# Optimization experiments

Hardware: AMD Instinct MI355X
Metric: run time of the kernel (lower is better)

The kernel has to match this reference:

```python
import jax, jax.numpy as jnp
import numpy as np

NS, NC = 16, 8  # n_state, n_ctrl; n_sc = NS + NC


def setup_inputs() -> dict:
    key = jax.random.key(0)
    kQ, kp, kF, kc, kx = jax.random.split(key, 5)
    B, T, nsc = 512, 128, NS + NC
    Qr = jax.random.normal(kQ, (B, T, nsc, nsc), dtype=jnp.float32)
    # PSD + regularized so Quu is invertible (as in the torch example: Q = Q^T Q)
    Q = jnp.einsum('btji,btjk->btik', Qr, Qr) / nsc + jnp.eye(nsc, dtype=jnp.float32)
    p = jax.random.normal(kp, (B, T, nsc), dtype=jnp.float32)
    F = jax.random.normal(kF, (B, T, NS, nsc), dtype=jnp.float32) * 0.3
    c1 = jax.random.normal(kc, (B, T, NS), dtype=jnp.float32)
    x_init = jax.random.normal(kx, (B, NS), dtype=jnp.float32)
    return {"Q": Q, "p": p, "F": F, "c1": c1, "x_init": x_init}


def _lqr(Q, p, F, c1, x_init):
    B, T, nsc = Q.shape[0], Q.shape[1], Q.shape[2]
    ns = F.shape[2]
    # time-major for scan: [T, B, ...]
    Qt = jnp.moveaxis(Q, 1, 0)
    pt = jnp.moveaxis(p, 1, 0)
    Ft = jnp.moveaxis(F, 1, 0)
    ct = jnp.moveaxis(c1, 1, 0)

    def bwd(carry, inp):
        V, v = carry                       # [B,ns,ns], [B,ns]
        Qc, pc, Fc, cc = inp
        # Q_t + F^T V F ; q_t + F^T V c1 + F^T v
        Qh = Qc + jnp.einsum('bni,bnm,bmj->bij', Fc, V, Fc)
        qh = pc + jnp.einsum('bni,bnm,bm->bi', Fc, V, cc) + jnp.einsum('bni,bn->bi', Fc, v)
        Qxx = Qh[:, :ns, :ns]
        Qxu = Qh[:, :ns, ns:]
        Qux = Qh[:, ns:, :ns]
        Quu = Qh[:, ns:, ns:]
        qx = qh[:, :ns]
        qu = qh[:, ns:]
        K = -jnp.linalg.solve(Quu, Qux)                    # [B,nc,ns]
        k = -jnp.linalg.solve(Quu, qu[..., None])[..., 0]  # [B,nc]
        KtQuu = jnp.einsum('bci,bcd->bid', K, Quu)
        Vn = Qxx + Qxu @ K + jnp.einsum('bci,bcj->bij', K, Qux) + KtQuu @ K
        Vn = 0.5 * (Vn + jnp.swapaxes(Vn, -1, -2))
        vn = qx + jnp.einsum('bic,bc->bi', Qxu, k) \
             + jnp.einsum('bci,bc->bi', K, qu) + jnp.einsum('bid,bd->bi', KtQuu, k)
        return (Vn, vn), (K, k)

    V0 = jnp.zeros((B, ns, ns), Q.dtype)
    v0 = jnp.zeros((B, ns), Q.dtype)
    _, (Ks, ks) = jax.lax.scan(bwd, (V0, v0), (Qt, pt, Ft, ct), reverse=True)

    def fwd(x, inp):
        K, k, Fc, cc = inp
        u = jnp.einsum('bci,bi->bc', K, x) + k
        tau = jnp.concatenate([x, u], axis=-1)             # [B, nsc]
        x_next = jnp.einsum('bnj,bj->bn', Fc, tau) + cc
        return x_next, tau

    _, taus = jax.lax.scan(fwd, x_init, (Ks, ks, Ft, ct))
    return jnp.moveaxis(taus, 0, 1)                        # [B, T, nsc]


def reference(Q, p, F, c1, x_init):
    return _lqr(Q, p, F, c1, x_init)
```

## Files before the change

### kernel.cpp

```cpp
#include <hip/hip_runtime.h>

namespace {
constexpr int TT = 128;

__device__ __forceinline__ float rdlane(float v, int l) {
  return __int_as_float(__builtin_amdgcn_readlane(__float_as_int(v), l));
}

__device__ __forceinline__ void bsync() {
  asm volatile("s_waitcnt lgkmcnt(0)" ::: "memory");
  __builtin_amdgcn_s_barrier();
  asm volatile("" ::: "memory");
  __builtin_amdgcn_sched_barrier(0);
}

__global__ __launch_bounds__(256)
void lqr_kernel(const float* __restrict__ Qg, const float* __restrict__ pg,
                const float* __restrict__ Fg, const float* __restrict__ cg,
                const float* __restrict__ x0g, float* __restrict__ out)
{
  __shared__ __align__(16) float VT[16][20];
  __shared__ __align__(16) float vv[16];
  __shared__ __align__(16) float FTxd[2][25][20];
  __shared__ __align__(16) float WTx[25][20];
  __shared__ __align__(16) float QhT[25][36];
  __shared__ __align__(16) float Ks[TT][16][8];
  __shared__ __align__(16) float ksv[TT][8];

  const int tid  = threadIdx.x;
  const int lane = tid & 63;
  const int wv   = tid >> 6;
  const int b    = blockIdx.x;
  const size_t bt0 = (size_t)b * TT;

  const int jl = tid & 31;
  const int g  = tid >> 5;

  for (int e = tid; e < 320; e += 256) (&VT[0][0])[e] = 0.f;
  if (tid < 16) vv[tid] = 0.f;

  const int  fj   = tid >> 2, fk = tid & 3;
  const bool fact = (tid < 100);
  const int  fsw  = (fj < 24) ? ((fj >> 2) & 3) : 2;
  float Fr4[4] = {0.f, 0.f, 0.f, 0.f};

  auto loadF = [&](int t) {
    if (fact) {
      if (fj < 24) {
        const float* Fs = Fg + (bt0 + t) * 384 + fj;
        #pragma unroll
        for (int m = 0; m < 4; ++m) Fr4[m] = Fs[(4 * fk + m) * 24];
      } else {
        const float* cs = cg + (bt0 + t) * 16 + 4 * fk;
        #pragma unroll
        for (int m = 0; m < 4; ++m) Fr4[m] = cs[m];
      }
    }
  };
  auto commitF = [&](int buf) {
    if (fact) {
      float* dst = &FTxd[buf][fj][(fk ^ fsw) << 2];
      *(float4*)dst = make_float4(Fr4[0], Fr4[1], Fr4[2], Fr4[3]);
    }
  };

  float qreg[3] = {0.f, 0.f, 0.f}, qreg3 = 0.f;
  auto loadQ = [&](int t) {
    if (jl < 24) {
      const float* Qs = Qg + (bt0 + t) * 576;
      #pragma unroll
      for (int r = 0; r < 3; ++r) qreg[r] = Qs[(3 * g + r) * 24 + jl];
      if (g == 7) qreg3 = pg[(bt0 + t) * 24 + jl];
    }
  };

  loadF(TT - 1);
  loadQ(TT - 1);
  commitF((TT - 1) & 1);
  loadF(TT - 2);
  bsync();

  for (int t = TT - 1; t >= 0; --t) {
    const float* Fb = &FTxd[t & 1][0][0];

    float fr[16];
    if (jl < 25) {
      const int sj = (jl >> 2) & 3;
      const float* fb = Fb + jl * 20;
      #pragma unroll
      for (int q = 0; q < 4; ++q) {
        float4 v4 = *(const float4*)(fb + ((q ^ sj) << 2));
        fr[4*q+0] = v4.x; fr[4*q+1] = v4.y; fr[4*q+2] = v4.z; fr[4*q+3] = v4.w;
      }
      const int m0 = 2 * g, m1 = m0 + 1;
      float acc0 = (jl == 24) ? vv[m0] : 0.f;
      float acc1 = (jl == 24) ? vv[m1] : 0.f;
      #pragma unroll
      for (int q = 0; q < 4; ++q) {
        float4 a0 = *(const float4*)(&VT[m0][4*q]);
        float4 a1 = *(const float4*)(&VT[m1][4*q]);
        acc0 = fmaf(a0.x, fr[4*q+0], acc0); acc0 = fmaf(a0.y, fr[4*q+1], acc0);
        acc0 = fmaf(a0.z, fr[4*q+2], acc0); acc0 = fmaf(a0.w, fr[4*q+3], acc0);
        acc1 = fmaf(a1.x, fr[4*q+0], acc1); acc1 = fmaf(a1.y, fr[4*q+1], acc1);
        acc1 = fmaf(a1.z, fr[4*q+2], acc1); acc1 = fmaf(a1.w, fr[4*q+3], acc1);
      }
      float* wb = &WTx[0][0] + jl * 20;
      *(float2*)(wb + ((((g >> 1) ^ sj) << 2) + (m0 & 3))) = make_float2(acc0, acc1);
    }
    bsync();

    if (jl < 24) {
      #pragma unroll
      for (int r = 0; r < 3; ++r) {
        const int c = 3 * g + r;
        const int sc = (c >> 2) & 3;
        const float* wb = &WTx[0][0] + c * 20;
        float acc = qreg[r];
        #pragma unroll
        for (int q = 0; q < 4; ++q) {
          float4 w4 = *(const float4*)(wb + ((q ^ sc) << 2));
          acc = fmaf(w4.x, fr[4*q+0], acc); acc = fmaf(w4.y, fr[4*q+1], acc);
          acc = fmaf(w4.z, fr[4*q+2], acc); acc = fmaf(w4.w, fr[4*q+3], acc);
        }
        float* qb = &QhT[0][0] + c * 36;
        qb[(((jl >> 2) ^ sc) << 2) + (jl & 3)] = acc;
      }
      if (g == 7) {
        const float* wb = &WTx[0][0] + 24 * 20;
        float acc = qreg3;
        #pragma unroll
        for (int q = 0; q < 4; ++q) {
          float4 w4 = *(const float4*)(wb + ((q ^ 2) << 2));
          acc = fmaf(w4.x, fr[4*q+0], acc); acc = fmaf(w4.y, fr[4*q+1], acc);
          acc = fmaf(w4.z, fr[4*q+2], acc); acc = fmaf(w4.w, fr[4*q+3], acc);
        }
        float* qb = &QhT[0][0] + 24 * 36;
        qb[(((jl >> 2) ^ 2) << 2) + (jl & 3)] = acc;
      }
    }
    if (t > 0) loadQ(t - 1);
    bsync();

    const int gjw = 2 + (t & 1);
    if (wv == gjw) {
      __builtin_amdgcn_s_setprio(1);
      const int cl = (lane < 25) ? lane : 0;
      const int row = (cl < 8) ? (16 + cl) : ((cl < 24) ? (cl - 8) : 24);
      const int s = (row >> 2) & 3;
      const float* base = &QhT[0][0] + row * 36;
      float a_[8];
      {
        float4 x0v = *(const float4*)(base + ((4 ^ s) << 2));
        float4 x1v = *(const float4*)(base + ((5 ^ s) << 2));
        a_[0]=x0v.x; a_[1]=x0v.y; a_[2]=x0v.z; a_[3]=x0v.w;
        a_[4]=x1v.x; a_[5]=x1v.y; a_[6]=x1v.z; a_[7]=x1v.w;
      }
      #pragma unroll
      for (int pp = 0; pp < 8; ++pp) {
        float f_[8];
        f_[0] = rdlane(a_[0], pp); f_[1] = rdlane(a_[1], pp);
        f_[2] = rdlane(a_[2], pp); f_[3] = rdlane(a_[3], pp);
        f_[4] = rdlane(a_[4], pp); f_[5] = rdlane(a_[5], pp);
        f_[6] = rdlane(a_[6], pp); f_[7] = rdlane(a_[7], pp);
        float d = __builtin_amdgcn_rcpf(f_[pp]);
        a_[pp] *= d;
        #pragma unroll
        for (int r = 0; r < 8; ++r)
          if (r != pp) a_[r] = fmaf(-f_[r], a_[pp], a_[r]);
      }
      if (lane >= 8 && lane < 25) {
        float4 k0 = make_float4(-a_[0], -a_[1], -a_[2], -a_[3]);
        float4 k1 = make_float4(-a_[4], -a_[5], -a_[6], -a_[7]);
        float4* kp = (lane < 24) ? (float4*)&Ks[t][lane - 8][0] : (float4*)&ksv[t][0];
        kp[0] = k0; kp[1] = k1;
      }
      const int jv = lane & 31;
      const int ih = lane >> 5;
      const int sl = (jv < 16) ? (8 + jv) : 24;
      float xj[8];
      #pragma unroll
      for (int c = 0; c < 8; ++c)
        xj[c] = __int_as_float(
            __builtin_amdgcn_ds_bpermute(sl * 4, __float_as_int(a_[c])));
      if (jv < 16 || jv == 24) {
        const int row2 = (jv < 16) ? jv : 24;
        const int s3 = (row2 >> 2) & 3;
        const float* b2 = &QhT[0][0] + row2 * 36;
        const int q0 = 2 * ih, q1 = q0 + 1;
        float4 A0 = *(const float4*)(b2 + ((q0 ^ s3) << 2));
        float4 A1 = *(const float4*)(b2 + ((q1 ^ s3) << 2));
        float acc[8];
        acc[0]=A0.x; acc[1]=A0.y; acc[2]=A0.z; acc[3]=A0.w;
        acc[4]=A1.x; acc[5]=A1.y; acc[6]=A1.z; acc[7]=A1.w;
        #pragma unroll
        for (int c = 0; c < 8; ++c) {
          const int s2 = ((16 + c) >> 2) & 3;
          const float* qb = &QhT[0][0] + (16 + c) * 36;
          float4 B0 = *(const float4*)(qb + ((q0 ^ s2) << 2));
          float4 B1 = *(const float4*)(qb + ((q1 ^ s2) << 2));
          const float xc = xj[c];
          acc[0] = fmaf(-xc, B0.x, acc[0]); acc[1] = fmaf(-xc, B0.y, acc[1]);
          acc[2] = fmaf(-xc, B0.z, acc[2]); acc[3] = fmaf(-xc, B0.w, acc[3]);
          acc[4] = fmaf(-xc, B1.x, acc[4]); acc[5] = fmaf(-xc, B1.y, acc[5]);
          acc[6] = fmaf(-xc, B1.z, acc[6]); acc[7] = fmaf(-xc, B1.w, acc[7]);
        }
        float4* vp = (jv < 16) ? (float4*)&VT[jv][8 * ih] : (float4*)&vv[8 * ih];
        vp[0] = make_float4(acc[0], acc[1], acc[2], acc[3]);
        vp[1] = make_float4(acc[4], acc[5], acc[6], acc[7]);
      }
      __builtin_amdgcn_s_setprio(0);
    } else {
      if (t > 0) commitF((t - 1) & 1);
      if (t > 1) loadF(t - 2);
    }
    bsync();
  }

  if (wv != 0) return;

  float xv = (lane < 16) ? x0g[(size_t)b * 16 + lane] : 0.f;
  float xs_[16];
  #pragma unroll
  for (int i = 0; i < 16; ++i) xs_[i] = rdlane(xv, i);

  float FA[24], FB[24];
  float cA = 0.f, cB = 0.f;
  float KA[16], KB[16], kA = 0.f, kB = 0.f;

  auto loadFw = [&](int t, float (&Fr)[24], float& cr) {
    if (lane < 16) {
      const float* src = Fg + (bt0 + t) * 384 + lane * 24;
      #pragma unroll
      for (int r = 0; r < 6; ++r) {
        float4 f4v = ((const float4*)src)[r];
        Fr[4*r+0] = f4v.x; Fr[4*r+1] = f4v.y; Fr[4*r+2] = f4v.z; Fr[4*r+3] = f4v.w;
      }
      cr = cg[(bt0 + t) * 16 + lane];
    }
  };
  auto loadK = [&](int t, float (&K)[16], float& kk) {
    if (lane < 8) {
      #pragma unroll
      for (int i = 0; i < 16; ++i) K[i] = Ks[t][i][lane];
      kk = ksv[t][lane];
    }
  };

  auto fstep = [&](int t, const float (&Fr)[24], float cr,
                   const float (&K)[16], float kk) {
    float uv = 0.f;
    if (lane < 8) {
      float u0 = kk, u1 = 0.f;
      #pragma unroll
      for (int i = 0; i < 16; i += 2) {
        u0 = fmaf(K[i],     xs_[i],     u0);
        u1 = fmaf(K[i + 1], xs_[i + 1], u1);
      }
      uv = u0 + u1;
    }
    float us[8];
    #pragma unroll
    for (int c = 0; c < 8; ++c) us[c] = rdlane(uv, c);
    float* o = out + (bt0 + t) * 24;
    if (lane < 16) o[lane] = xv;
    if (lane < 8)  o[16 + lane] = uv;
    float x0a = cr, x1a = 0.f;
    #pragma unroll
    for (int j2 = 0; j2 < 16; j2 += 2) {
      x0a = fmaf(Fr[j2],     xs_[j2],     x0a);
      x1a = fmaf(Fr[j2 + 1], xs_[j2 + 1], x1a);
    }
    #pragma unroll
    for (int c = 0; c < 8; c += 2) {
      x0a = fmaf(Fr[16 + c],     us[c],     x0a);
      x1a = fmaf(Fr[16 + c + 1], us[c + 1], x1a);
    }
    xv = x0a + x1a;
    #pragma unroll
    for (int i = 0; i < 16; ++i) xs_[i] = rdlane(xv, i);
  };

  loadFw(0, FA, cA); loadK(0, KA, kA);
  for (int t = 0; t < TT; t += 2) {
    if (t + 1 < TT) { loadFw(t + 1, FB, cB); loadK(t + 1, KB, kB); }
    fstep(t, FA, cA, KA, kA);
    if (t + 2 < TT) { loadFw(t + 2, FA, cA); loadK(t + 2, KA, kA); }
    fstep(t + 1, FB, cB, KB, kB);
  }
}
}

extern "C" void kernel_launch(void* const* d_in, const int* in_sizes, int n_in,
                              void* d_out, int out_size, void* d_ws, size_t ws_size,
                              hipStream_t stream)
{
  (void)n_in; (void)out_size; (void)d_ws; (void)ws_size;
  const float* Q  = (const float*)d_in[0];
  const float* p  = (const float*)d_in[1];
  const float* F  = (const float*)d_in[2];
  const float* c1 = (const float*)d_in[3];
  const float* x0 = (const float*)d_in[4];
  float* outp = (float*)d_out;

  const int B = in_sizes[4] / 16;
  lqr_kernel<<<B, 256, 0, stream>>>(Q, p, F, c1, x0, outp);
}
```

Measured before the change: 282.9 us.

## Pack two batch chains per block with staggered phases sharing barriers

Each 512-thread block now processes two batch elements with separate shared-memory state. The second chain runs one phase behind the first, so the latency-bound Gauss-Jordan phase of one chain overlaps the matmul phases of the other within the same barrier intervals. The intent is to hide the serial per-timestep solve latency and halve the number of barrier rounds per batch. In exchange, shared memory per block roughly doubles, the grid is halved, and the extra skew adds one phase to the schedule; the code also assumes an even batch count.

Result: slower. 355.9 us (+25.8%).

```diff
diff --git a/kernel.cpp b/kernel.cpp
--- a/kernel.cpp
+++ b/kernel.cpp
@@ -14,35 +14,39 @@
   __builtin_amdgcn_sched_barrier(0);
 }
 
-__global__ __launch_bounds__(256)
+__global__ __launch_bounds__(512)
 void lqr_kernel(const float* __restrict__ Qg, const float* __restrict__ pg,
                 const float* __restrict__ Fg, const float* __restrict__ cg,
                 const float* __restrict__ x0g, float* __restrict__ out)
 {
-  __shared__ __align__(16) float VT[16][20];
-  __shared__ __align__(16) float vv[16];
-  __shared__ __align__(16) float FTxd[2][25][20];
-  __shared__ __align__(16) float WTx[25][20];
-  __shared__ __align__(16) float QhT[25][36];
-  __shared__ __align__(16) float Ks[TT][16][8];
-  __shared__ __align__(16) float ksv[TT][8];
+  __shared__ __align__(16) float VT[2][16][20];
+  __shared__ __align__(16) float vv[2][16];
+  __shared__ __align__(16) float FTxd[2][2][25][20];
+  __shared__ __align__(16) float WTx[2][25][20];
+  __shared__ __align__(16) float QhT[2][25][36];
+  __shared__ __align__(16) float Ks[2][TT][16][8];
+  __shared__ __align__(16) float ksv[2][TT][8];
 
   const int tid  = threadIdx.x;
-  const int lane = tid & 63;
-  const int wv   = tid >> 6;
-  const int b    = blockIdx.x;
-  const size_t bt0 = (size_t)b * TT;
-
-  const int jl = tid & 31;
-  const int g  = tid >> 5;
-
-  for (int e = tid; e < 320; e += 256) (&VT[0][0])[e] = 0.f;
-  if (tid < 16) vv[tid] = 0.f;
-
-  const int  fj   = tid >> 2, fk = tid & 3;
-  const bool fact = (tid < 100);
+  const int cid  = tid >> 8;
+  const int ctid = tid & 255;
+  const int lane = ctid & 63;
+  const int cwv  = ctid >> 6;
+  const int b2   = blockIdx.x * 2 + cid;
+  const size_t bt0 = (size_t)b2 * TT;
+
+  const int jl = ctid & 31;
+  const int g  = ctid >> 5;
+
+  for (int e = ctid; e < 320; e += 256) (&VT[cid][0][0])[e] = 0.f;
+  if (ctid < 16) vv[cid][ctid] = 0.f;
+
+  const int  fj   = ctid >> 2, fk = ctid & 3;
+  const bool fact = (ctid < 100);
   const int  fsw  = (fj < 24) ? ((fj >> 2) & 3) : 2;
   float Fr4[4] = {0.f, 0.f, 0.f, 0.f};
+  float qreg[3] = {0.f, 0.f, 0.f}, qreg3 = 0.f;
+  float fr[16];
 
   auto loadF = [&](int t) {
     if (fact) {
@@ -59,12 +63,10 @@
   };
   auto commitF = [&](int buf) {
     if (fact) {
-      float* dst = &FTxd[buf][fj][(fk ^ fsw) << 2];
+      float* dst = &FTxd[cid][buf][fj][(fk ^ fsw) << 2];
       *(float4*)dst = make_float4(Fr4[0], Fr4[1], Fr4[2], Fr4[3]);
     }
   };
-
-  float qreg[3] = {0.f, 0.f, 0.f}, qreg3 = 0.f;
   auto loadQ = [&](int t) {
     if (jl < 24) {
       const float* Qs = Qg + (bt0 + t) * 576;
@@ -74,16 +76,8 @@
     }
   };
 
-  loadF(TT - 1);
-  loadQ(TT - 1);
-  commitF((TT - 1) & 1);
-  loadF(TT - 2);
-  bsync();
-
-  for (int t = TT - 1; t >= 0; --t) {
-    const float* Fb = &FTxd[t & 1][0][0];
-
-    float fr[16];
+  auto phaseA = [&](int t) {
+    const float* Fb = &FTxd[cid][t & 1][0][0];
     if (jl < 25) {
       const int sj = (jl >> 2) & 3;
       const float* fb = Fb + jl * 20;
@@ -93,28 +87,29 @@
         fr[4*q+0] = v4.x; fr[4*q+1] = v4.y; fr[4*q+2] = v4.z; fr[4*q+3] = v4.w;
       }
       const int m0 = 2 * g, m1 = m0 + 1;
-      float acc0 = (jl == 24) ? vv[m0] : 0.f;
-      float acc1 = (jl == 24) ? vv[m1] : 0.f;
+      float acc0 = (jl == 24) ? vv[cid][m0] : 0.f;
+      float acc1 = (jl == 24) ? vv[cid][m1] : 0.f;
       #pragma unroll
       for (int q = 0; q < 4; ++q) {
-        float4 a0 = *(const float4*)(&VT[m0][4*q]);
-        float4 a1 = *(const float4*)(&VT[m1][4*q]);
+        float4 a0 = *(const float4*)(&VT[cid][m0][4*q]);
+        float4 a1 = *(const float4*)(&VT[cid][m1][4*q]);
         acc0 = fmaf(a0.x, fr[4*q+0], acc0); acc0 = fmaf(a0.y, fr[4*q+1], acc0);
         acc0 = fmaf(a0.z, fr[4*q+2], acc0); acc0 = fmaf(a0.w, fr[4*q+3], acc0);
         acc1 = fmaf(a1.x, fr[4*q+0], acc1); acc1 = fmaf(a1.y, fr[4*q+1], acc1);
         acc1 = fmaf(a1.z, fr[4*q+2], acc1); acc1 = fmaf(a1.w, fr[4*q+3], acc1);
       }
-      float* wb = &WTx[0][0] + jl * 20;
+      float* wb = &WTx[cid][0][0] + jl * 20;
       *(float2*)(wb + ((((g >> 1) ^ sj) << 2) + (m0 & 3))) = make_float2(acc0, acc1);
     }
-    bsync();
-
+  };
+
+  auto phaseB = [&](int t) {
     if (jl < 24) {
       #pragma unroll
       for (int r = 0; r < 3; ++r) {
         const int c = 3 * g + r;
         const int sc = (c >> 2) & 3;
-        const float* wb = &WTx[0][0] + c * 20;
+        const float* wb = &WTx[cid][0][0] + c * 20;
         float acc = qreg[r];
         #pragma unroll
         for (int q = 0; q < 4; ++q) {
@@ -122,11 +117,11 @@
           acc = fmaf(w4.x, fr[4*q+0], acc); acc = fmaf(w4.y, fr[4*q+1], acc);
           acc = fmaf(w4.z, fr[4*q+2], acc); acc = fmaf(w4.w, fr[4*q+3], acc);
         }
-        float* qb = &QhT[0][0] + c * 36;
+        float* qb = &QhT[cid][0][0] + c * 36;
         qb[(((jl >> 2) ^ sc) << 2) + (jl & 3)] = acc;
       }
       if (g == 7) {
-        const float* wb = &WTx[0][0] + 24 * 20;
+        const float* wb = &WTx[cid][0][0] + 24 * 20;
         float acc = qreg3;
         #pragma unroll
         for (int q = 0; q < 4; ++q) {
@@ -134,91 +129,116 @@
           acc = fmaf(w4.x, fr[4*q+0], acc); acc = fmaf(w4.y, fr[4*q+1], acc);
           acc = fmaf(w4.z, fr[4*q+2], acc); acc = fmaf(w4.w, fr[4*q+3], acc);
         }
-        float* qb = &QhT[0][0] + 24 * 36;
+        float* qb = &QhT[cid][0][0] + 24 * 36;
         qb[(((jl >> 2) ^ 2) << 2) + (jl & 3)] = acc;
       }
     }
     if (t > 0) loadQ(t - 1);
+  };
+
+  auto phaseG = [&](int tg) {
+    if (cwv != 2 + (tg & 1)) return;
+    __builtin_amdgcn_s_setprio(1);
+    const int cl = (lane < 25) ? lane : 0;
+    const int row = (cl < 8) ? (16 + cl) : ((cl < 24) ? (cl - 8) : 24);
+    const int s = (row >> 2) & 3;
+    const float* base = &QhT[cid][0][0] + row * 36;
+    float a_[8];
+    {
+      float4 x0v = *(const float4*)(base + ((4 ^ s) << 2));
+      float4 x1v = *(const float4*)(base + ((5 ^ s) << 2));
+      a_[0]=x0v.x; a_[1]=x0v.y; a_[2]=x0v.z; a_[3]=x0v.w;
+      a_[4]=x1v.x; a_[5]=x1v.y; a_[6]=x1v.z; a_[7]=x1v.w;
+    }
+    #pragma unroll
+    for (int pp = 0; pp < 8; ++pp) {
+      float f_[8];
+      f_[0] = rdlane(a_[0], pp); f_[1] = rdlane(a_[1], pp);
+      f_[2] = rdlane(a_[2], pp); f_[3] = rdlane(a_[3], pp);
+      f_[4] = rdlane(a_[4], pp); f_[5] = rdlane(a_[5], pp);
+      f_[6] = rdlane(a_[6], pp); f_[7] = rdlane(a_[7], pp);
+      float d = __builtin_amdgcn_rcpf(f_[pp]);
+      a_[pp] *= d;
+      #pragma unroll
+      for (int r = 0; r < 8; ++r)
+        if (r != pp) a_[r] = fmaf(-f_[r], a_[pp], a_[r]);
+    }
+    if (lane >= 8 && lane < 25) {
+      float4 k0 = make_float4(-a_[0], -a_[1], -a_[2], -a_[3]);
+      float4 k1 = make_float4(-a_[4], -a_[5], -a_[6], -a_[7]);
+      float4* kp = (lane < 24) ? (float4*)&Ks[cid][tg][lane - 8][0]
+                               : (float4*)&ksv[cid][tg][0];
+      kp[0] = k0; kp[1] = k1;
+    }
+    const int jv = lane & 31;
+    const int ih = lane >> 5;
+    const int sl = (jv < 16) ? (8 + jv) : 24;
+    float xj[8];
+    #pragma unroll
+    for (int c = 0; c < 8; ++c)
+      xj[c] = __int_as_float(
+          __builtin_amdgcn_ds_bpermute(sl * 4, __float_as_int(a_[c])));
+    if (jv < 16 || jv == 24) {
+      const int row2 = (jv < 16) ? jv : 24;
+      const int s3 = (row2 >> 2) & 3;
+      const float* b2p = &QhT[cid][0][0] + row2 * 36;
+      const int q0 = 2 * ih, q1 = q0 + 1;
+      float4 A0 = *(const float4*)(b2p + ((q0 ^ s3) << 2));
+      float4 A1 = *(const float4*)(b2p + ((q1 ^ s3) << 2));
+      float acc[8];
+      acc[0]=A0.x; acc[1]=A0.y; acc[2]=A0.z; acc[3]=A0.w;
+      acc[4]=A1.x; acc[5]=A1.y; acc[6]=A1.z; acc[7]=A1.w;
+      #pragma unroll
+      for (int c = 0; c < 8; ++c) {
+        const int s2 = ((16 + c) >> 2) & 3;
+        const float* qb = &QhT[cid][0][0] + (16 + c) * 36;
+        float4 B0 = *(const float4*)(qb + ((q0 ^ s2) << 2));
+        float4 B1 = *(const float4*)(qb + ((q1 ^ s2) << 2));
+        const float xc = xj[c];
+        acc[0] = fmaf(-xc, B0.x, acc[0]); acc[1] = fmaf(-xc, B0.y, acc[1]);
+        acc[2] = fmaf(-xc, B0.z, acc[2]); acc[3] = fmaf(-xc, B0.w, acc[3]);
+        acc[4] = fmaf(-xc, B1.x, acc[4]); acc[5] = fmaf(-xc, B1.y, acc[5]);
+        acc[6] = fmaf(-xc, B1.z, acc[6]); acc[7] = fmaf(-xc, B1.w, acc[7]);
+      }
+      float4* vp = (jv < 16) ? (float4*)&VT[cid][jv][8 * ih]
+                             : (float4*)&vv[cid][8 * ih];
+      vp[0] = make_float4(acc[0], acc[1], acc[2], acc[3]);
+      vp[1] = make_float4(acc[4], acc[5], acc[6], acc[7]);
+    }
+    __builtin_amdgcn_s_setprio(0);
+  };
+
+  loadF(TT - 1);
+  loadQ(TT - 1);
+  if (cid == 0) { commitF(1); loadF(TT - 2); }
+  bsync();
+
+  for (int t = TT - 1; t >= 0; --t) {
+    if (cid == 0) {
+      phaseA(t);
+    } else {
+      if (t + 1 < TT) phaseG(t + 1);
+      commitF(t & 1);
+      if (t > 0) loadF(t - 1);
+    }
     bsync();
-
-    const int gjw = 2 + (t & 1);
-    if (wv == gjw) {
-      __builtin_amdgcn_s_setprio(1);
-      const int cl = (lane < 25) ? lane : 0;
-      const int row = (cl < 8) ? (16 + cl) : ((cl < 24) ? (cl - 8) : 24);
-      const int s = (row >> 2) & 3;
-      const float* base = &QhT[0][0] + row * 36;
-      float a_[8];
-      {
-        float4 x0v = *(const float4*)(base + ((4 ^ s) << 2));
-        float4 x1v = *(const float4*)(base + ((5 ^ s) << 2));
-        a_[0]=x0v.x; a_[1]=x0v.y; a_[2]=x0v.z; a_[3]=x0v.w;
-        a_[4]=x1v.x; a_[5]=x1v.y; a_[6]=x1v.z; a_[7]=x1v.w;
-      }
-      #pragma unroll
-      for (int pp = 0; pp < 8; ++pp) {
-        float f_[8];
-        f_[0] = rdlane(a_[0], pp); f_[1] = rdlane(a_[1], pp);
-        f_[2] = rdlane(a_[2], pp); f_[3] = rdlane(a_[3], pp);
-        f_[4] = rdlane(a_[4], pp); f_[5] = rdlane(a_[5], pp);
-        f_[6] = rdlane(a_[6], pp); f_[7] = rdlane(a_[7], pp);
-        float d = __builtin_amdgcn_rcpf(f_[pp]);
-        a_[pp] *= d;
-        #pragma unroll
-        for (int r = 0; r < 8; ++r)
-          if (r != pp) a_[r] = fmaf(-f_[r], a_[pp], a_[r]);
-      }
-      if (lane >= 8 && lane < 25) {
-        float4 k0 = make_float4(-a_[0], -a_[1], -a_[2], -a_[3]);
-        float4 k1 = make_float4(-a_[4], -a_[5], -a_[6], -a_[7]);
-        float4* kp = (lane < 24) ? (float4*)&Ks[t][lane - 8][0] : (float4*)&ksv[t][0];
-        kp[0] = k0; kp[1] = k1;
-      }
-      const int jv = lane & 31;
-      const int ih = lane >> 5;
-      const int sl = (jv < 16) ? (8 + jv) : 24;
-      float xj[8];
-      #pragma unroll
-      for (int c = 0; c < 8; ++c)
-        xj[c] = __int_as_float(
-            __builtin_amdgcn_ds_bpermute(sl * 4, __float_as_int(a_[c])));
-      if (jv < 16 || jv == 24) {
-        const int row2 = (jv < 16) ? jv : 24;
-        const int s3 = (row2 >> 2) & 3;
-        const float* b2 = &QhT[0][0] + row2 * 36;
-        const int q0 = 2 * ih, q1 = q0 + 1;
-        float4 A0 = *(const float4*)(b2 + ((q0 ^ s3) << 2));
-        float4 A1 = *(const float4*)(b2 + ((q1 ^ s3) << 2));
-        float acc[8];
-        acc[0]=A0.x; acc[1]=A0.y; acc[2]=A0.z; acc[3]=A0.w;
-        acc[4]=A1.x; acc[5]=A1.y; acc[6]=A1.z; acc[7]=A1.w;
-        #pragma unroll
-        for (int c = 0; c < 8; ++c) {
-          const int s2 = ((16 + c) >> 2) & 3;
-          const float* qb = &QhT[0][0] + (16 + c) * 36;
-          float4 B0 = *(const float4*)(qb + ((q0 ^ s2) << 2));
-          float4 B1 = *(const float4*)(qb + ((q1 ^ s2) << 2));
-          const float xc = xj[c];
-          acc[0] = fmaf(-xc, B0.x, acc[0]); acc[1] = fmaf(-xc, B0.y, acc[1]);
-          acc[2] = fmaf(-xc, B0.z, acc[2]); acc[3] = fmaf(-xc, B0.w, acc[3]);
-          acc[4] = fmaf(-xc, B1.x, acc[4]); acc[5] = fmaf(-xc, B1.y, acc[5]);
-          acc[6] = fmaf(-xc, B1.z, acc[6]); acc[7] = fmaf(-xc, B1.w, acc[7]);
-        }
-        float4* vp = (jv < 16) ? (float4*)&VT[jv][8 * ih] : (float4*)&vv[8 * ih];
-        vp[0] = make_float4(acc[0], acc[1], acc[2], acc[3]);
-        vp[1] = make_float4(acc[4], acc[5], acc[6], acc[7]);
-      }
-      __builtin_amdgcn_s_setprio(0);
-    } else {
+    if (cid == 0) phaseB(t); else phaseA(t);
+    bsync();
+    if (cid == 0) {
+      phaseG(t);
       if (t > 0) commitF((t - 1) & 1);
       if (t > 1) loadF(t - 2);
+    } else {
+      phaseB(t);
     }
     bsync();
   }
-
-  if (wv != 0) return;
-
-  float xv = (lane < 16) ? x0g[(size_t)b * 16 + lane] : 0.f;
+  if (cid == 1) phaseG(0);
+  bsync();
+
+  if (cwv != 0) return;
+
+  float xv = (lane < 16) ? x0g[(size_t)b2 * 16 + lane] : 0.f;
   float xs_[16];
   #pragma unroll
   for (int i = 0; i < 16; ++i) xs_[i] = rdlane(xv, i);
@@ -241,8 +261,8 @@
   auto loadK = [&](int t, float (&K)[16], float& kk) {
     if (lane < 8) {
       #pragma unroll
-      for (int i = 0; i < 16; ++i) K[i] = Ks[t][i][lane];
-      kk = ksv[t][lane];
+      for (int i = 0; i < 16; ++i) K[i] = Ks[cid][t][i][lane];
+      kk = ksv[cid][t][lane];
     }
   };
 
@@ -303,5 +323,5 @@
   float* outp = (float*)d_out;
 
   const int B = in_sizes[4] / 16;
-  lqr_kernel<<<B, 256, 0, stream>>>(Q, p, F, c1, x0, outp);
-}
+  lqr_kernel<<<B / 2, 512, 0, stream>>>(Q, p, F, c1, x0, outp);
+}
```

## Split the per-step Quu solve and V update redundantly across all four waves

Applied to the files above, without the earlier changes.

Previously one alternating wave did the 8x8 Gauss-Jordan solve and the full 16x16 V update while the other waves staged F. Now all four waves redo the small solve redundantly, and each wave computes a 4-column slice of the V/v update with B operands prefetched before the solve. F commit and prefetch move ahead of the solve in every wave. This shortens the serial critical path of each time step, but every wave now does the solve and the F staging in every step, which may add contention.

New measurement: 294.2 us. 1.04x slower.

```diff
diff --git a/kernel.cpp b/kernel.cpp
--- a/kernel.cpp
+++ b/kernel.cpp
@@ -76,7 +76,7 @@
 
   loadF(TT - 1);
   loadQ(TT - 1);
-  commitF((TT - 1) & 1);
+  commitF(1);
   loadF(TT - 2);
   bsync();
 
@@ -141,9 +141,10 @@
     if (t > 0) loadQ(t - 1);
     bsync();
 
-    const int gjw = 2 + (t & 1);
-    if (wv == gjw) {
-      __builtin_amdgcn_s_setprio(1);
+    {
+      if (t > 0) commitF((t - 1) & 1);
+      if (t > 1) loadF(t - 2);
+
       const int cl = (lane < 25) ? lane : 0;
       const int row = (cl < 8) ? (16 + cl) : ((cl < 24) ? (cl - 8) : 24);
       const int s = (row >> 2) & 3;
@@ -155,6 +156,25 @@
         a_[0]=x0v.x; a_[1]=x0v.y; a_[2]=x0v.z; a_[3]=x0v.w;
         a_[4]=x1v.x; a_[5]=x1v.y; a_[6]=x1v.z; a_[7]=x1v.w;
       }
+
+      const int jv = (lane < 25) ? lane : 0;
+      const bool vact = (lane < 25) && ((jv < 16) || (jv == 24));
+      const int row2 = (jv < 16) ? jv : 24;
+      const int s3 = (row2 >> 2) & 3;
+      float4 A0 = *(const float4*)(&QhT[0][0] + row2 * 36 + ((wv ^ s3) << 2));
+      float4 Bv0, Bv1, Bv2, Bv3, Bv4, Bv5, Bv6, Bv7;
+      {
+        const float* q16 = &QhT[0][0];
+        Bv0 = *(const float4*)(q16 + 16 * 36 + ((wv ^ 0) << 2));
+        Bv1 = *(const float4*)(q16 + 17 * 36 + ((wv ^ 0) << 2));
+        Bv2 = *(const float4*)(q16 + 18 * 36 + ((wv ^ 0) << 2));
+        Bv3 = *(const float4*)(q16 + 19 * 36 + ((wv ^ 0) << 2));
+        Bv4 = *(const float4*)(q16 + 20 * 36 + ((wv ^ 1) << 2));
+        Bv5 = *(const float4*)(q16 + 21 * 36 + ((wv ^ 1) << 2));
+        Bv6 = *(const float4*)(q16 + 22 * 36 + ((wv ^ 1) << 2));
+        Bv7 = *(const float4*)(q16 + 23 * 36 + ((wv ^ 1) << 2));
+      }
+
       #pragma unroll
       for (int pp = 0; pp < 8; ++pp) {
         float f_[8];
@@ -168,50 +188,43 @@
         for (int r = 0; r < 8; ++r)
           if (r != pp) a_[r] = fmaf(-f_[r], a_[pp], a_[r]);
       }
-      if (lane >= 8 && lane < 25) {
+
+      if (wv == 3 && lane >= 8 && lane < 25) {
         float4 k0 = make_float4(-a_[0], -a_[1], -a_[2], -a_[3]);
         float4 k1 = make_float4(-a_[4], -a_[5], -a_[6], -a_[7]);
-        float4* kp = (lane < 24) ? (float4*)&Ks[t][lane - 8][0] : (float4*)&ksv[t][0];
+        float4* kp = (lane < 24) ? (float4*)&Ks[t][lane - 8][0]
+                                 : (float4*)&ksv[t][0];
         kp[0] = k0; kp[1] = k1;
       }
-      const int jv = lane & 31;
-      const int ih = lane >> 5;
+
       const int sl = (jv < 16) ? (8 + jv) : 24;
       float xj[8];
       #pragma unroll
       for (int c = 0; c < 8; ++c)
         xj[c] = __int_as_float(
             __builtin_amdgcn_ds_bpermute(sl * 4, __float_as_int(a_[c])));
-      if (jv < 16 || jv == 24) {
-        const int row2 = (jv < 16) ? jv : 24;
-        const int s3 = (row2 >> 2) & 3;
-        const float* b2 = &QhT[0][0] + row2 * 36;
-        const int q0 = 2 * ih, q1 = q0 + 1;
-        float4 A0 = *(const float4*)(b2 + ((q0 ^ s3) << 2));
-        float4 A1 = *(const float4*)(b2 + ((q1 ^ s3) << 2));
-        float acc[8];
-        acc[0]=A0.x; acc[1]=A0.y; acc[2]=A0.z; acc[3]=A0.w;
-        acc[4]=A1.x; acc[5]=A1.y; acc[6]=A1.z; acc[7]=A1.w;
-        #pragma unroll
-        for (int c = 0; c < 8; ++c) {
-          const int s2 = ((16 + c) >> 2) & 3;
-          const float* qb = &QhT[0][0] + (16 + c) * 36;
-          float4 B0 = *(const float4*)(qb + ((q0 ^ s2) << 2));
-          float4 B1 = *(const float4*)(qb + ((q1 ^ s2) << 2));
-          const float xc = xj[c];
-          acc[0] = fmaf(-xc, B0.x, acc[0]); acc[1] = fmaf(-xc, B0.y, acc[1]);
-          acc[2] = fmaf(-xc, B0.z, acc[2]); acc[3] = fmaf(-xc, B0.w, acc[3]);
-          acc[4] = fmaf(-xc, B1.x, acc[4]); acc[5] = fmaf(-xc, B1.y, acc[5]);
-          acc[6] = fmaf(-xc, B1.z, acc[6]); acc[7] = fmaf(-xc, B1.w, acc[7]);
-        }
-        float4* vp = (jv < 16) ? (float4*)&VT[jv][8 * ih] : (float4*)&vv[8 * ih];
-        vp[0] = make_float4(acc[0], acc[1], acc[2], acc[3]);
-        vp[1] = make_float4(acc[4], acc[5], acc[6], acc[7]);
-      }
-      __builtin_amdgcn_s_setprio(0);
-    } else {
-      if (t > 0) commitF((t - 1) & 1);
-      if (t > 1) loadF(t - 2);
+      if (vact) {
+        float acc[4];
+        acc[0] = A0.x; acc[1] = A0.y; acc[2] = A0.z; acc[3] = A0.w;
+        acc[0] = fmaf(-xj[0], Bv0.x, acc[0]); acc[1] = fmaf(-xj[0], Bv0.y, acc[1]);
+        acc[2] = fmaf(-xj[0], Bv0.z, acc[2]); acc[3] = fmaf(-xj[0], Bv0.w, acc[3]);
+        acc[0] = fmaf(-xj[1], Bv1.x, acc[0]); acc[1] = fmaf(-xj[1], Bv1.y, acc[1]);
+        acc[2] = fmaf(-xj[1], Bv1.z, acc[2]); acc[3] = fmaf(-xj[1], Bv1.w, acc[3]);
+        acc[0] = fmaf(-xj[2], Bv2.x, acc[0]); acc[1] = fmaf(-xj[2], Bv2.y, acc[1]);
+        acc[2] = fmaf(-xj[2], Bv2.z, acc[2]); acc[3] = fmaf(-xj[2], Bv2.w, acc[3]);
+        acc[0] = fmaf(-xj[3], Bv3.x, acc[0]); acc[1] = fmaf(-xj[3], Bv3.y, acc[1]);
+        acc[2] = fmaf(-xj[3], Bv3.z, acc[2]); acc[3] = fmaf(-xj[3], Bv3.w, acc[3]);
+        acc[0] = fmaf(-xj[4], Bv4.x, acc[0]); acc[1] = fmaf(-xj[4], Bv4.y, acc[1]);
+        acc[2] = fmaf(-xj[4], Bv4.z, acc[2]); acc[3] = fmaf(-xj[4], Bv4.w, acc[3]);
+        acc[0] = fmaf(-xj[5], Bv5.x, acc[0]); acc[1] = fmaf(-xj[5], Bv5.y, acc[1]);
+        acc[2] = fmaf(-xj[5], Bv5.z, acc[2]); acc[3] = fmaf(-xj[5], Bv5.w, acc[3]);
+        acc[0] = fmaf(-xj[6], Bv6.x, acc[0]); acc[1] = fmaf(-xj[6], Bv6.y, acc[1]);
+        acc[2] = fmaf(-xj[6], Bv6.z, acc[2]); acc[3] = fmaf(-xj[6], Bv6.w, acc[3]);
+        acc[0] = fmaf(-xj[7], Bv7.x, acc[0]); acc[1] = fmaf(-xj[7], Bv7.y, acc[1]);
+        acc[2] = fmaf(-xj[7], Bv7.z, acc[2]); acc[3] = fmaf(-xj[7], Bv7.w, acc[3]);
+        float* vp = (jv < 16) ? &VT[jv][4 * wv] : &vv[4 * wv];
+        *(float4*)vp = make_float4(acc[0], acc[1], acc[2], acc[3]);
+      }
     }
     bsync();
   }
```
